# Performance work log

Hardware: AMD Instinct MI355X
Metric: run time of the kernel (lower is better)

## Reference

```python
import jax, jax.numpy as jnp
import numpy as np
from functools import partial

B, H, W, C = 16, 64, 64, 512      # images, feature H, feature W, channels
R = 256                            # raw RPN proposals per image (sorted by objectness)
N_REGIONS = 64                     # regions kept after NMS
PH, PW = 7, 7                      # pool_size (h, w)
IOU_THR = 0.4
FH, FW = H, W                      # feature_size (h, w)
NEG = -jnp.inf


def _nms_indices(roi):
    # roi: [R, 4] (x, y, w, h). Scores are descending by construction
    # (tf.reverse(tf.range(n)/n)), so greedy NMS processes rows in order.
    x, y, w, h = roi[:, 0], roi[:, 1], roi[:, 2], roi[:, 3]
    y1, x1, y2, x2 = y, x, y + h, x + w
    area = (y2 - y1) * (x2 - x1)
    ih = jnp.maximum(jnp.minimum(y2[:, None], y2[None, :]) - jnp.maximum(y1[:, None], y1[None, :]), 0.0)
    iw = jnp.maximum(jnp.minimum(x2[:, None], x2[None, :]) - jnp.maximum(x1[:, None], x1[None, :]), 0.0)
    inter = ih * iw
    union = area[:, None] + area[None, :] - inter
    iou = jnp.where(union > 0, inter / union, 0.0)  # [R, R]

    def step(keep, xs):
        i, row = xs
        suppressed = jnp.any(keep & (row > IOU_THR))
        return keep.at[i].set(~suppressed), None

    keep, _ = jax.lax.scan(step, jnp.zeros((R,), bool), (jnp.arange(R), iou))
    rank = jnp.cumsum(keep.astype(jnp.int32)) - 1
    valid = keep & (rank < N_REGIONS)
    # Unfilled slot j gets tail index R - N_REGIONS + j, which is exactly
    # tf.concat([nms, tf.range(n_roi)[size(nms) - n_regions:]], 0).
    fill = R - N_REGIONS + jnp.arange(N_REGIONS)
    idx = fill.at[jnp.where(valid, rank, N_REGIONS)].set(jnp.arange(R), mode='drop')
    return idx


def _fix_axis(mn, mx, ps, fs):
    pad = ps - (mx - mn)
    fix_min = mn < pad // 2
    fix_max = fs - mx < (1 + pad) // 2
    symmetric = (pad > 0) & ~(fix_min | fix_max)
    omin = jnp.where(symmetric, mn - pad // 2, mn)
    omax = jnp.where(symmetric, mx + (1 + pad) // 2, mx)
    omin = jnp.where((pad > 0) & fix_min, 0, omin)
    omax = jnp.where((pad > 0) & fix_min, ps, omax)
    omin = jnp.where((pad > 0) & fix_max, fs - ps, omin)
    omax = jnp.where((pad > 0) & fix_max, fs, omax)
    return omin, omax


def _clip_roi(roi):
    # roi: [B, N_REGIONS, 4] float (x, y, w, h) -> int32 clipped (x, y, w, h)
    x_min = jnp.maximum(0.0, roi[..., 0]).astype(jnp.int32)
    y_min = jnp.maximum(0.0, roi[..., 1]).astype(jnp.int32)
    x_max = jnp.minimum(float(FW), roi[..., 0] + roi[..., 2]).astype(jnp.int32)
    y_max = jnp.minimum(float(FH), roi[..., 1] + roi[..., 3]).astype(jnp.int32)
    x_min, x_max = _fix_axis(x_min, x_max, PW, FW)   # x axis uses si=1 (width)
    y_min, y_max = _fix_axis(y_min, y_max, PH, FH)   # y axis uses si=0 (height)
    return jnp.stack([x_min, y_min, x_max - x_min, y_max - y_min], axis=-1)


def _pool_one(fm, r):
    # fm: [H, W, C]; r: int32 (x, y, w, h).
    # Faithful to the traced tf.function behaviour of _pool_roi: region.shape[0]
    # is dynamic (None) so region_shape = pool_size, hence h_step = w_step = 1:
    # bins i < PH-1 are single rows y+i; the last bin spans rows [y+PH-1, y+h).
    x, y, w, h = r[0], r[1], r[2], r[3]
    ii = y + jnp.arange(PH - 1)
    jj = x + jnp.arange(PW - 1)
    rmask = (jnp.arange(H) >= y + PH - 1) & (jnp.arange(H) < y + h)
    cmask = (jnp.arange(W) >= x + PW - 1) & (jnp.arange(W) < x + w)
    block = fm[ii[:, None], jj[None, :], :]                                   # [PH-1, PW-1, C]
    col_strip = jnp.max(jnp.where(cmask[None, :, None], fm, NEG), axis=1)     # [H, C]
    corner = jnp.max(jnp.where(rmask[:, None], col_strip, NEG), axis=0)       # [C]
    row_strip = jnp.max(jnp.where(rmask[:, None, None], fm[:, jj, :], NEG), axis=0)  # [PW-1, C]
    top = jnp.concatenate([block, col_strip[ii][:, None, :]], axis=1)         # [PH-1, PW, C]
    bottom = jnp.concatenate([row_strip, corner[None, :]], axis=0)[None]      # [1, PW, C]
    return jnp.concatenate([top, bottom], axis=0)                             # [PH, PW, C]


def _forward(features, roi):
    idx = jax.vmap(_nms_indices)(roi)                           # [B, N_REGIONS]
    roi_nms = jnp.take_along_axis(roi, idx[..., None], axis=1)  # [B, N_REGIONS, 4]
    roi_clipped = _clip_roi(roi_nms)                            # int32 [B, N_REGIONS, 4]
    pooled = jax.vmap(lambda fm, rs: jax.vmap(partial(_pool_one, fm))(rs))(features, roi_clipped)
    return pooled, roi_clipped


def setup_inputs():
    key = jax.random.key(0)
    k1, k2, k3 = jax.random.split(key, 3)
    features = jax.random.normal(k1, (B, H, W, C), dtype=jnp.float32)
    xy = jax.random.uniform(k2, (B, R, 2), dtype=jnp.float32) * 60.0
    wh = jax.random.uniform(k3, (B, R, 2), dtype=jnp.float32) * 30.0 + 2.0
    roi = jnp.concatenate([xy, wh], axis=-1)
    return {"features": features, "roi": roi}


def reference(features, roi):
    return _forward(features, roi)
```

## Files before the change

kernel.cpp:

```cpp
#include <hip/hip_runtime.h>
#include <math.h>

namespace {
constexpr int kB = 16, kH = 64, kW = 64, kC = 512;
constexpr int kR = 256, kN = 64, kPH = 7, kPW = 7;
constexpr int kC4 = kC / 4;
constexpr float kIouThr = 0.4f;
constexpr size_t kPooledElems = (size_t)kB * kN * kPH * kPW * kC;
}

__device__ __forceinline__ float4 max4(float4 a, float4 b) {
    return make_float4(fmaxf(a.x, b.x), fmaxf(a.y, b.y),
                       fmaxf(a.z, b.z), fmaxf(a.w, b.w));
}

__global__ __launch_bounds__(256) void nms_clip_kernel(
        const float* __restrict__ roi, float* __restrict__ out_roi) {
    const int b = blockIdx.x;
    const int tid = threadIdx.x;
    const float* r = roi + (size_t)b * kR * 4;

    __shared__ float4 box[kR];
    __shared__ float area[kR];
    __shared__ unsigned long long M[kR][4];
    __shared__ unsigned long long kw[4];
    __shared__ int idx[kN];

    if (tid < kN) idx[tid] = kR - kN + tid;

    const float4 rr = ((const float4*)r)[tid];
    const float x1 = rr.x, y1 = rr.y, x2 = rr.x + rr.z, y2 = rr.y + rr.w;
    box[tid] = make_float4(x1, y1, x2, y2);
    area[tid] = (y2 - y1) * (x2 - x1);
    __syncthreads();

    {
        unsigned long long m0 = 0, m1 = 0, m2 = 0, m3 = 0;
        const float ai = area[tid];
        for (int j = 0; j < kR; ++j) {
            const float4 bj = box[j];
            const float ih = fmaxf(fminf(y2, bj.w) - fmaxf(y1, bj.y), 0.0f);
            const float iw = fmaxf(fminf(x2, bj.z) - fmaxf(x1, bj.x), 0.0f);
            const float inter = ih * iw;
            const float uni = ai + area[j] - inter;
            const float iou = (uni > 0.0f) ? (inter / uni) : 0.0f;
            if (iou > kIouThr) {
                const unsigned long long bit = 1ull << (j & 63);
                if ((j >> 6) == 0) m0 |= bit;
                else if ((j >> 6) == 1) m1 |= bit;
                else if ((j >> 6) == 2) m2 |= bit;
                else m3 |= bit;
            }
        }
        M[tid][0] = m0; M[tid][1] = m1; M[tid][2] = m2; M[tid][3] = m3;
    }
    __syncthreads();

    if (tid == 0) {
        unsigned long long s0 = 0, s1 = 0, s2 = 0, s3 = 0;
        unsigned long long k0 = 0, k1 = 0, k2 = 0, k3 = 0;
        unsigned long long n0 = M[0][0], n1 = M[0][1], n2 = M[0][2], n3 = M[0][3];
#pragma unroll
        for (int wi = 0; wi < 4; ++wi) {
            for (int bi = 0; bi < 64; ++bi) {
                const unsigned long long m0 = n0, m1 = n1, m2 = n2, m3 = n3;
                const int ip = (wi * 64 + bi + 1) & 255;
                n0 = M[ip][0]; n1 = M[ip][1]; n2 = M[ip][2]; n3 = M[ip][3];
                const unsigned long long sw =
                    (wi == 0) ? s0 : (wi == 1) ? s1 : (wi == 2) ? s2 : s3;
                if (!((sw >> bi) & 1ull)) {
                    const unsigned long long bit = 1ull << bi;
                    if (wi == 0) k0 |= bit;
                    else if (wi == 1) k1 |= bit;
                    else if (wi == 2) k2 |= bit;
                    else k3 |= bit;
                    s0 |= m0; s1 |= m1; s2 |= m2; s3 |= m3;
                }
            }
        }
        kw[0] = k0; kw[1] = k1; kw[2] = k2; kw[3] = k3;
    }
    __syncthreads();

    {
        const int wi = tid >> 6, bi = tid & 63;
        const unsigned long long kwv = kw[wi];
        if ((kwv >> bi) & 1ull) {
            int rank = 0;
            for (int w2 = 0; w2 < wi; ++w2) rank += __popcll(kw[w2]);
            const unsigned long long below =
                (bi == 0) ? 0ull : (~0ull >> (64 - bi));
            rank += __popcll(kwv & below);
            if (rank < kN) idx[rank] = tid;
        }
    }
    __syncthreads();

    if (tid < kN) {
        const int i = idx[tid];
        const float x = r[i * 4 + 0], y = r[i * 4 + 1];
        const float w = r[i * 4 + 2], h = r[i * 4 + 3];
        int x_min = (int)fmaxf(0.0f, x);
        int y_min = (int)fmaxf(0.0f, y);
        int x_max = (int)fminf((float)kW, x + w);
        int y_max = (int)fminf((float)kH, y + h);
        {
            const int pad = kPW - (x_max - x_min);
            const bool fmn = x_min < (pad >> 1);
            const bool fmx = (kW - x_max) < ((1 + pad) >> 1);
            const bool sym = (pad > 0) && !(fmn || fmx);
            int omin = sym ? (x_min - (pad >> 1)) : x_min;
            int omax = sym ? (x_max + ((1 + pad) >> 1)) : x_max;
            if ((pad > 0) && fmn) { omin = 0; omax = kPW; }
            if ((pad > 0) && fmx) { omin = kW - kPW; omax = kW; }
            x_min = omin; x_max = omax;
        }
        {
            const int pad = kPH - (y_max - y_min);
            const bool fmn = y_min < (pad >> 1);
            const bool fmx = (kH - y_max) < ((1 + pad) >> 1);
            const bool sym = (pad > 0) && !(fmn || fmx);
            int omin = sym ? (y_min - (pad >> 1)) : y_min;
            int omax = sym ? (y_max + ((1 + pad) >> 1)) : y_max;
            if ((pad > 0) && fmn) { omin = 0; omax = kPH; }
            if ((pad > 0) && fmx) { omin = kH - kPH; omax = kH; }
            y_min = omin; y_max = omax;
        }
        float4 rf;
        rf.x = (float)x_min; rf.y = (float)y_min;
        rf.z = (float)(x_max - x_min); rf.w = (float)(y_max - y_min);
        ((float4*)out_roi)[b * kN + tid] = rf;
    }
}

__global__ __launch_bounds__(512) void pool_kernel(
        const float4* __restrict__ fm4, const float4* __restrict__ rcf,
        float4* __restrict__ out4) {
    const int rid = blockIdx.x;
    const int b = rid >> 6;
    const int tid = threadIdx.x;
    const int s = tid >> 7;
    const int t = tid & 127;
    const float4 rf = rcf[rid];
    const int x = (int)rf.x, y = (int)rf.y;
    const int w = (int)rf.z, h = (int)rf.w;

    const float4* fm = fm4 + (size_t)b * kH * kW * kC4;
    float4* out = out4 + (size_t)rid * (kPH * kPW) * kC4;

    const float NI = -__builtin_inff();
    const float4 ninf = make_float4(NI, NI, NI, NI);

    for (int p = s; p < 6; p += 4) {
        const float4* row = fm + (size_t)(y + p) * kW * kC4 + t;
#pragma unroll
        for (int q = 0; q < 6; ++q) {
            out[(p * 7 + q) * kC4 + t] = row[(size_t)(x + q) * kC4];
        }
        float4 m = ninf;
        for (int j = x + 6; j < x + w; ++j) {
            m = max4(m, row[(size_t)j * kC4]);
        }
        out[(p * 7 + 6) * kC4 + t] = m;
    }

    float4 pm[7];
#pragma unroll
    for (int o = 0; o < 7; ++o) pm[o] = ninf;
    for (int i = y + 6 + s; i < y + h; i += 4) {
        const float4* row = fm + (size_t)i * kW * kC4 + t;
#pragma unroll
        for (int q = 0; q < 6; ++q) {
            pm[q] = max4(pm[q], row[(size_t)(x + q) * kC4]);
        }
        float4 c = pm[6];
        for (int j = x + 6; j < x + w; ++j) {
            c = max4(c, row[(size_t)j * kC4]);
        }
        pm[6] = c;
    }

    __shared__ float4 red[3][7][128];
    if (s > 0) {
#pragma unroll
        for (int o = 0; o < 7; ++o) red[s - 1][o][t] = pm[o];
    }
    __syncthreads();
    if (s == 0) {
#pragma unroll
        for (int o = 0; o < 7; ++o) {
            float4 v = pm[o];
            v = max4(v, red[0][o][t]);
            v = max4(v, red[1][o][t]);
            v = max4(v, red[2][o][t]);
            out[(42 + o) * kC4 + t] = v;
        }
    }
}

extern "C" void kernel_launch(void* const* d_in, const int* in_sizes, int n_in,
                              void* d_out, int out_size, void* d_ws, size_t ws_size,
                              hipStream_t stream) {
    (void)in_sizes; (void)n_in; (void)d_ws; (void)ws_size; (void)out_size;
    const float* features = (const float*)d_in[0];
    const float* roi = (const float*)d_in[1];
    float* out = (float*)d_out;
    float* out_roi = out + kPooledElems;

    nms_clip_kernel<<<kB, 256, 0, stream>>>(roi, out_roi);
    pool_kernel<<<kB * kN, 512, 0, stream>>>(
        (const float4*)features, (const float4*)out_roi, (float4*)out);
}
```

Before: 347.5 us.

## Split pool blocks by channel half, swizzle block order, unroll column max

Each RoI now gets two 256-thread blocks, each covering half of the channels, which doubles the grid and raises occupancy (launch bounds 256, 7). Block IDs are remapped by blockIdx&7 so that consecutive RoIs land on the same XCD, aiming for better L2 reuse of feature maps. The column-max loops use four independent accumulators to expose more memory-level parallelism. The cost is more blocks that each do less work, plus a permuted block ordering.

```diff
diff --git a/kernel.cpp b/kernel.cpp
--- a/kernel.cpp
+++ b/kernel.cpp
@@ -5,6 +5,7 @@
 constexpr int kB = 16, kH = 64, kW = 64, kC = 512;
 constexpr int kR = 256, kN = 64, kPH = 7, kPW = 7;
 constexpr int kC4 = kC / 4;
+constexpr int kG = 64;
 constexpr float kIouThr = 0.4f;
 constexpr size_t kPooledElems = (size_t)kB * kN * kPH * kPW * kC;
 }
@@ -133,54 +134,72 @@
     }
 }
 
-__global__ __launch_bounds__(512) void pool_kernel(
+__global__ __launch_bounds__(256, 7) void pool_kernel(
         const float4* __restrict__ fm4, const float4* __restrict__ rcf,
         float4* __restrict__ out4) {
-    const int rid = blockIdx.x;
+    constexpr int kNBlk = kB * kN * 2;
+    constexpr int kCpx = kNBlk / 8;
+    const int bid = (blockIdx.x & 7) * kCpx + (blockIdx.x >> 3);
+    const int rid = bid >> 1;
+    const int half = bid & 1;
     const int b = rid >> 6;
     const int tid = threadIdx.x;
-    const int s = tid >> 7;
-    const int t = tid & 127;
+    const int s = tid >> 6;
+    const int t = tid & 63;
+    const int g = half * kG + t;
+
     const float4 rf = rcf[rid];
     const int x = (int)rf.x, y = (int)rf.y;
     const int w = (int)rf.z, h = (int)rf.w;
 
-    const float4* fm = fm4 + (size_t)b * kH * kW * kC4;
-    float4* out = out4 + (size_t)rid * (kPH * kPW) * kC4;
+    const float4* fm = fm4 + (size_t)b * kH * kW * kC4 + g;
+    float4* out = out4 + (size_t)rid * (kPH * kPW) * kC4 + g;
 
     const float NI = -__builtin_inff();
     const float4 ninf = make_float4(NI, NI, NI, NI);
 
     for (int p = s; p < 6; p += 4) {
-        const float4* row = fm + (size_t)(y + p) * kW * kC4 + t;
-#pragma unroll
-        for (int q = 0; q < 6; ++q) {
-            out[(p * 7 + q) * kC4 + t] = row[(size_t)(x + q) * kC4];
-        }
-        float4 m = ninf;
-        for (int j = x + 6; j < x + w; ++j) {
-            m = max4(m, row[(size_t)j * kC4]);
-        }
-        out[(p * 7 + 6) * kC4 + t] = m;
+        const float4* row = fm + ((y + p) * kW + x) * kC4;
+        float4 v0 = row[0 * kC4], v1 = row[1 * kC4], v2 = row[2 * kC4];
+        float4 v3 = row[3 * kC4], v4 = row[4 * kC4], v5 = row[5 * kC4];
+        out[(p * 7 + 0) * kC4] = v0;
+        out[(p * 7 + 1) * kC4] = v1;
+        out[(p * 7 + 2) * kC4] = v2;
+        out[(p * 7 + 3) * kC4] = v3;
+        out[(p * 7 + 4) * kC4] = v4;
+        out[(p * 7 + 5) * kC4] = v5;
+        float4 m0 = ninf, m1 = ninf, m2 = ninf, m3 = ninf;
+        int j = 6;
+        for (; j + 4 <= w; j += 4) {
+            float4 a0 = row[(j + 0) * kC4], a1 = row[(j + 1) * kC4];
+            float4 a2 = row[(j + 2) * kC4], a3 = row[(j + 3) * kC4];
+            m0 = max4(m0, a0); m1 = max4(m1, a1);
+            m2 = max4(m2, a2); m3 = max4(m3, a3);
+        }
+        for (; j < w; ++j) m0 = max4(m0, row[j * kC4]);
+        out[(p * 7 + 6) * kC4] = max4(max4(m0, m1), max4(m2, m3));
     }
 
     float4 pm[7];
 #pragma unroll
     for (int o = 0; o < 7; ++o) pm[o] = ninf;
     for (int i = y + 6 + s; i < y + h; i += 4) {
-        const float4* row = fm + (size_t)i * kW * kC4 + t;
-#pragma unroll
-        for (int q = 0; q < 6; ++q) {
-            pm[q] = max4(pm[q], row[(size_t)(x + q) * kC4]);
-        }
-        float4 c = pm[6];
-        for (int j = x + 6; j < x + w; ++j) {
-            c = max4(c, row[(size_t)j * kC4]);
-        }
-        pm[6] = c;
-    }
-
-    __shared__ float4 red[3][7][128];
+        const float4* row = fm + (i * kW + x) * kC4;
+#pragma unroll
+        for (int q = 0; q < 6; ++q) pm[q] = max4(pm[q], row[q * kC4]);
+        float4 c0 = pm[6], c1 = ninf, c2 = ninf, c3 = ninf;
+        int j = 6;
+        for (; j + 4 <= w; j += 4) {
+            float4 a0 = row[(j + 0) * kC4], a1 = row[(j + 1) * kC4];
+            float4 a2 = row[(j + 2) * kC4], a3 = row[(j + 3) * kC4];
+            c0 = max4(c0, a0); c1 = max4(c1, a1);
+            c2 = max4(c2, a2); c3 = max4(c3, a3);
+        }
+        for (; j < w; ++j) c0 = max4(c0, row[j * kC4]);
+        pm[6] = max4(max4(c0, c1), max4(c2, c3));
+    }
+
+    __shared__ float4 red[3][kPH][kG];
     if (s > 0) {
 #pragma unroll
         for (int o = 0; o < 7; ++o) red[s - 1][o][t] = pm[o];
@@ -193,7 +212,7 @@
             v = max4(v, red[0][o][t]);
             v = max4(v, red[1][o][t]);
             v = max4(v, red[2][o][t]);
-            out[(42 + o) * kC4 + t] = v;
+            out[(42 + o) * kC4] = v;
         }
     }
 }
@@ -208,6 +227,6 @@
     float* out_roi = out + kPooledElems;
 
     nms_clip_kernel<<<kB, 256, 0, stream>>>(roi, out_roi);
-    pool_kernel<<<kB * kN, 512, 0, stream>>>(
+    pool_kernel<<<kB * kN * 2, 256, 0, stream>>>(
         (const float4*)features, (const float4*)out_roi, (float4*)out);
 }
```

Result: no change. 351.0 us (+1.0%).
